# Optimization experiments

Hardware: AMD Instinct MI355X
Metric: run time of the kernel (lower is better)

## Reference

```python
import jax, jax.numpy as jnp
import numpy as np

BETA = 100.0
EXTS = [("r1", 515, 32, 16), ("r1_1", 512, 32, 16), ("r2", 512, 48, 12), ("r2_2", 576, 48, 12),
        ("r3", 576, 64, 12), ("r3_3", 768, 96, 8), ("r4", 768, 128, 6), ("r4_4", 768, 160, 6),
        ("r5", 960, 192, 5), ("r5_5", 960, 224, 4)]


def _wn(v, g):
    # torch weight_norm(dim=0): w[o] = g[o] * v[o] / ||v[o]||  (norm over input dims)
    n = jnp.sqrt(jnp.sum(v * v, axis=-1, keepdims=True))
    return g[..., None] * v / n


def _softplus_b(z):
    # torch Softplus(beta): (1/beta) * log(1 + exp(beta*z))
    return jax.nn.softplus(BETA * z) / BETA


def _resnext(x, grad, v, g, b):
    # x: [B,Cin,N], grad: [B,N,Cin,3]; v: [L,c,Cin] -- L parallel 1x1-conv branches,
    # outputs concatenated along channels (each branch reads the SAME input x).
    w = _wn(v, g)                                             # [L,c,Cin]
    pre = jnp.einsum('lci,bin->blcn', w, x) + b[None, :, :, None]
    sg = jax.nn.sigmoid(BETA * pre)                           # softplus' = sigmoid(beta*pre)
    B, L, c, N = pre.shape
    x_out = _softplus_b(pre).reshape(B, L * c, N)
    g_out = jnp.einsum('lci,bnid->bnlcd', w, grad)            # analytic chain-rule matmul
    g_out = (sg.transpose(0, 3, 1, 2)[..., None] * g_out).reshape(B, N, L * c, 3)
    return x_out, g_out


def setup_inputs() -> dict:
    key = jax.random.key(0)
    ks = iter(jax.random.split(key, 64))
    B, N = 1, 4096
    d = {}
    d["input"] = jax.random.normal(next(ks), (B, N, 3), jnp.float32)
    d["latent"] = jax.random.normal(next(ks), (B, 256), jnp.float32) * 0.1
    d["c1_v"] = jax.random.normal(next(ks), (515, 259), jnp.float32) * np.float32(np.sqrt(2.0 / 259.0))
    d["c1_g"] = 1.0 + 0.01 * jax.random.normal(next(ks), (515,), jnp.float32)
    d["c1_b"] = jnp.zeros((515,), jnp.float32)
    for name, cin, c, L in EXTS:
        d[name + "_v"] = jax.random.normal(next(ks), (L, c, cin), jnp.float32) * np.float32(np.sqrt(2.0 / cin))
        d[name + "_g"] = 1.0 + 0.01 * jax.random.normal(next(ks), (L, c), jnp.float32)
        d[name + "_b"] = jnp.zeros((L, c), jnp.float32)
    d["c10_v"] = jax.random.normal(next(ks), (1, 896), jnp.float32) * 1e-4 + np.float32(np.sqrt(np.pi / 896.0))
    d["c10_g"] = 1.0 + 0.01 * jax.random.normal(next(ks), (1,), jnp.float32)
    d["c10_b"] = -jnp.ones((1,), jnp.float32)
    return d


def reference(input, latent, c1_v, c1_g, c1_b,
              r1_v, r1_g, r1_b, r1_1_v, r1_1_g, r1_1_b,
              r2_v, r2_g, r2_b, r2_2_v, r2_2_g, r2_2_b,
              r3_v, r3_g, r3_b, r3_3_v, r3_3_g, r3_3_b,
              r4_v, r4_g, r4_b, r4_4_v, r4_4_g, r4_4_b,
              r5_v, r5_g, r5_b, r5_5_v, r5_5_g, r5_5_b,
              c10_v, c10_g, c10_b):
    # ImplicitMap_fExtrator.forward with compute_grad=True, cat_latent=True
    B, N = input.shape[0], input.shape[1]
    lat = jnp.broadcast_to(latent[:, None, :], (B, N, latent.shape[-1]))
    input_con = jnp.concatenate([input, lat], axis=-1)        # [B,N,259]
    x = input_con.transpose(0, 2, 1)                           # [B,259,N]

    # first conv: is_first=True -> input grad = w[:, :3] (d/d xyz)
    w1 = _wn(c1_v, c1_g)                                       # [515,259]
    pre = jnp.einsum('ci,bin->bcn', w1, x) + c1_b[None, :, None]
    grad = jnp.broadcast_to(w1[:, :3][None, None, :, :], (B, N, 515, 3))
    grad = jax.nn.sigmoid(BETA * pre).transpose(0, 2, 1)[..., None] * grad
    x = _softplus_b(pre)

    ext_params = [(r1_v, r1_g, r1_b), (r1_1_v, r1_1_g, r1_1_b),
                  (r2_v, r2_g, r2_b), (r2_2_v, r2_2_g, r2_2_b),
                  (r3_v, r3_g, r3_b), (r3_3_v, r3_3_g, r3_3_b),
                  (r4_v, r4_g, r4_b), (r4_4_v, r4_4_g, r4_4_b),
                  (r5_v, r5_g, r5_b), (r5_5_v, r5_5_g, r5_5_b)]
    for v, g, b in ext_params:
        x, grad = _resnext(x, grad, v, g, b)

    w10 = _wn(c10_v, c10_g)                                    # [1,896]
    out = jnp.einsum('ci,bin->bcn', w10, x) + c10_b[None, :, None]  # [B,1,N]
    out_grad = jnp.einsum('ci,bnid->bncd', w10, grad)               # [B,N,1,3]
    return out, out_grad, input_con
```

## Files before the change

kernel.cpp:

```cpp
#include <hip/hip_runtime.h>
#include <hip/hip_bf16.h>


#define NPTS 4096
#define XS 968

typedef unsigned short u16;
typedef unsigned int   u32;
typedef __attribute__((ext_vector_type(8))) __bf16 bf16x8;
typedef __attribute__((ext_vector_type(4))) float  f32x4;

__device__ __forceinline__ float bf2f(u16 h) {
  return __uint_as_float(((u32)h) << 16);
}
__device__ __forceinline__ u16 f2bf(float f) {
  u32 u = __float_as_uint(f);
  u += 0x7fff + ((u >> 16) & 1);
  return (u16)(u >> 16);
}

__device__ __forceinline__ void act_sp_sg(float pre, float& sp, float& sg) {
  float z = 100.f * pre;
  float e = __expf(-fabsf(z));
  float r = 1.f / (1.f + e);
  float l = __logf(1.f + e) * 0.01f;
  if (z >= 0.f) { sg = r;       sp = pre + l; }
  else          { sg = 1.f - r; sp = l; }
}

__global__ __launch_bounds__(256)
void build_x0(const float* __restrict__ inp, const float* __restrict__ lat,
              u16* __restrict__ x0, float* __restrict__ con) {
  const int n = blockIdx.x;
  for (int i = threadIdx.x; i < 320; i += 256) {
    float v = (i < 3) ? inp[n * 3 + i] : ((i < 259) ? lat[i - 3] : 0.f);
    x0[(size_t)n * 320 + i] = f2bf(v);
    if (i < 259) con[(size_t)n * 259 + i] = v;
  }
}

struct WLayer { const float* v; const float* g; int Cin, Cout, KS, MF; size_t woff; };
struct WAll { WLayer L[11]; };

__global__ __launch_bounds__(256)
void wnormF(WAll wa, u16* __restrict__ Wf) {
  const WLayer L = wa.L[blockIdx.y];
  const int cb = blockIdx.x;
  if (cb >= L.MF) return;
  __shared__ float red[16][17];
  __shared__ float scl[16];
  const int t = threadIdx.x;
  {
    const int col16 = t & 15, kt = t >> 4;
    const int col = cb * 16 + col16;
    float ss = 0.f;
    if (col < L.Cout)
      for (int k = kt; k < L.Cin; k += 16) {
        float x = L.v[(size_t)col * L.Cin + k]; ss += x * x;
      }
    red[col16][kt] = ss;
  }
  __syncthreads();
  if (t < 16) {
    float s = 0.f;
#pragma unroll
    for (int j = 0; j < 16; ++j) s += red[t][j];
    const int c = cb * 16 + t;
    scl[t] = (c < L.Cout) ? L.g[c] / sqrtf(s) : 0.f;
  }
  __syncthreads();
  u32* dst = (u32*)(Wf + L.woff);
  const int lane = t >> 2, q = t & 3;
  const int vcol = cb * 16 + (lane & 15);
  const float sc = scl[lane & 15];
  const float* vrow = L.v + (size_t)vcol * L.Cin;
  const bool cok = vcol < L.Cout;
  for (int ks = 0; ks < L.KS; ++ks) {
    const int k0 = ks * 32 + (lane >> 4) * 8 + q * 2;
    u16 lo = 0, hi16 = 0;
    if (cok) {
      if (k0 < L.Cin)     lo   = f2bf(vrow[k0] * sc);
      if (k0 + 1 < L.Cin) hi16 = f2bf(vrow[k0 + 1] * sc);
    }
    dst[(size_t)(ks * L.MF + cb) * 128 + t] = (u32)lo | ((u32)hi16 << 16);
  }
}

struct FusedArgs {
  size_t woff[11];
  const float* bias[11];
  const float* v10; const float* g10; const float* b10;
};

template<int KS, int MF, int COUT>
__device__ __forceinline__ void layer_mid(const u16* __restrict__ Wf,
                                          const float* __restrict__ bias,
                                          u16* __restrict__ X,
                                          int w, int lane, int lcol, int hi) {
  constexpr int NF = (MF + 11) / 12;
  f32x4 acc[4][NF];
#pragma unroll
  for (int s = 0; s < 4; ++s)
#pragma unroll
    for (int i = 0; i < NF; ++i) acc[s][i] = (f32x4){0.f, 0.f, 0.f, 0.f};

  const u16* wp = Wf + lane * 8;
  const int abase = lcol * XS + hi * 8;
  bf16x8 bA[NF], bB[NF];
#pragma unroll
  for (int i = 0; i < NF; ++i)
    if (w + 12 * i < MF)
      bA[i] = *(const bf16x8*)(wp + (size_t)(w + 12 * i) * 512);

#pragma unroll 1
  for (int ks = 0; ks < KS; ks += 2) {
    bf16x8 af[4];
#pragma unroll
    for (int s = 0; s < 4; ++s)
      af[s] = *(const bf16x8*)(X + abase + s * 16 * XS + ks * 32);
#pragma unroll
    for (int i = 0; i < NF; ++i)
      if (w + 12 * i < MF)
        bB[i] = *(const bf16x8*)(wp + (size_t)((ks + 1) * MF + w + 12 * i) * 512);
#pragma unroll
    for (int i = 0; i < NF; ++i)
      if (w + 12 * i < MF)
#pragma unroll
        for (int s = 0; s < 4; ++s)
          acc[s][i] = __builtin_amdgcn_mfma_f32_16x16x32_bf16(af[s], bA[i], acc[s][i], 0, 0, 0);
#pragma unroll
    for (int s = 0; s < 4; ++s)
      af[s] = *(const bf16x8*)(X + abase + s * 16 * XS + ks * 32 + 32);
    if (ks + 2 < KS) {
#pragma unroll
      for (int i = 0; i < NF; ++i)
        if (w + 12 * i < MF)
          bA[i] = *(const bf16x8*)(wp + (size_t)((ks + 2) * MF + w + 12 * i) * 512);
    }
#pragma unroll
    for (int i = 0; i < NF; ++i)
      if (w + 12 * i < MF)
#pragma unroll
        for (int s = 0; s < 4; ++s)
          acc[s][i] = __builtin_amdgcn_mfma_f32_16x16x32_bf16(af[s], bB[i], acc[s][i], 0, 0, 0);
  }
  __syncthreads();
#pragma unroll
  for (int i = 0; i < NF; ++i) {
    const int cb = w + 12 * i;
    if (cb < MF) {
      const int col = cb * 16 + lcol;
      const bool ok = col < COUT;
      const float bc = ok ? bias[col] : 0.f;
#pragma unroll
      for (int r = 0; r < 4; ++r) {
        const int p = hi * 4 + r;
        float sp = 0.f, sg = 0.f;
        if (ok) act_sp_sg(acc[0][i][r] + bc, sp, sg);
        X[(0 * 16 + p) * XS + col] = f2bf(sp);
        X[(1 * 16 + p) * XS + col] = f2bf(ok ? sg * acc[1][i][r] : 0.f);
        X[(2 * 16 + p) * XS + col] = f2bf(ok ? sg * acc[2][i][r] : 0.f);
        X[(3 * 16 + p) * XS + col] = f2bf(ok ? sg * acc[3][i][r] : 0.f);
      }
    }
  }
  __syncthreads();
}

template<int KS, int MF, int COUT>
__device__ __forceinline__ void layer_first(const u16* __restrict__ Wf,
                                            const float* __restrict__ bias,
                                            u16* __restrict__ X,
                                            int w, int lane, int lcol, int hi) {
  constexpr int NF = (MF + 11) / 12;
  f32x4 acc[NF];
#pragma unroll
  for (int i = 0; i < NF; ++i) acc[i] = (f32x4){0.f, 0.f, 0.f, 0.f};
  const u16* wp = Wf + lane * 8;
  const int abase = lcol * XS + hi * 8;
  bf16x8 bA[NF], bB[NF];
#pragma unroll
  for (int i = 0; i < NF; ++i)
    if (w + 12 * i < MF)
      bA[i] = *(const bf16x8*)(wp + (size_t)(w + 12 * i) * 512);
#pragma unroll 1
  for (int ks = 0; ks < KS; ks += 2) {
    bf16x8 af0 = *(const bf16x8*)(X + abase + ks * 32);
#pragma unroll
    for (int i = 0; i < NF; ++i)
      if (w + 12 * i < MF)
        bB[i] = *(const bf16x8*)(wp + (size_t)((ks + 1) * MF + w + 12 * i) * 512);
#pragma unroll
    for (int i = 0; i < NF; ++i)
      if (w + 12 * i < MF)
        acc[i] = __builtin_amdgcn_mfma_f32_16x16x32_bf16(af0, bA[i], acc[i], 0, 0, 0);
    bf16x8 af1 = *(const bf16x8*)(X + abase + ks * 32 + 32);
    if (ks + 2 < KS) {
#pragma unroll
      for (int i = 0; i < NF; ++i)
        if (w + 12 * i < MF)
          bA[i] = *(const bf16x8*)(wp + (size_t)((ks + 2) * MF + w + 12 * i) * 512);
    }
#pragma unroll
    for (int i = 0; i < NF; ++i)
      if (w + 12 * i < MF)
        acc[i] = __builtin_amdgcn_mfma_f32_16x16x32_bf16(af1, bB[i], acc[i], 0, 0, 0);
  }
  __syncthreads();
#pragma unroll
  for (int i = 0; i < NF; ++i) {
    const int cb = w + 12 * i;
    if (cb < MF) {
      const int col = cb * 16 + lcol;
      const bool ok = col < COUT;
      float bc = 0.f, w0 = 0.f, w1 = 0.f, w2 = 0.f;
      if (ok) {
        bc = bias[col];
        const u16* wk = Wf + ((size_t)cb * 64 + lcol) * 8;
        w0 = bf2f(wk[0]); w1 = bf2f(wk[1]); w2 = bf2f(wk[2]);
      }
#pragma unroll
      for (int r = 0; r < 4; ++r) {
        const int p = hi * 4 + r;
        float sp = 0.f, sg = 0.f;
        if (ok) act_sp_sg(acc[i][r] + bc, sp, sg);
        X[(0 * 16 + p) * XS + col] = f2bf(sp);
        X[(1 * 16 + p) * XS + col] = f2bf(sg * w0);
        X[(2 * 16 + p) * XS + col] = f2bf(sg * w1);
        X[(3 * 16 + p) * XS + col] = f2bf(sg * w2);
      }
    }
  }
  __syncthreads();
}

__global__ __launch_bounds__(768, 1)
void fused_net(FusedArgs fa, const u16* __restrict__ WfAll,
               const u16* __restrict__ x0,
               float* __restrict__ out, float* __restrict__ outg) {
  __shared__ __align__(16) u16 X[64 * XS];
  __shared__ float fred[12];
  const int t = threadIdx.x;
  const int w = t >> 6, lane = t & 63;
  const int lcol = lane & 15, hi = lane >> 4;
  const int n0 = blockIdx.x * 16;

  for (int c = t; c < 640; c += 768) {
    const int row = c / 40, ch = c % 40;
    uint4 q = *reinterpret_cast<const uint4*>(x0 + (size_t)(n0 + row) * 320 + ch * 8);
    *reinterpret_cast<uint4*>(X + row * XS + ch * 8) = q;
  }
  __syncthreads();

  layer_first<10, 36, 515>(WfAll + fa.woff[0],  fa.bias[0],  X, w, lane, lcol, hi);
  layer_mid<18, 32, 512>(WfAll + fa.woff[1],  fa.bias[1],  X, w, lane, lcol, hi);
  layer_mid<16, 32, 512>(WfAll + fa.woff[2],  fa.bias[2],  X, w, lane, lcol, hi);
  layer_mid<16, 36, 576>(WfAll + fa.woff[3],  fa.bias[3],  X, w, lane, lcol, hi);
  layer_mid<18, 36, 576>(WfAll + fa.woff[4],  fa.bias[4],  X, w, lane, lcol, hi);
  layer_mid<18, 48, 768>(WfAll + fa.woff[5],  fa.bias[5],  X, w, lane, lcol, hi);
  layer_mid<24, 48, 768>(WfAll + fa.woff[6],  fa.bias[6],  X, w, lane, lcol, hi);
  layer_mid<24, 48, 768>(WfAll + fa.woff[7],  fa.bias[7],  X, w, lane, lcol, hi);
  layer_mid<24, 60, 960>(WfAll + fa.woff[8],  fa.bias[8],  X, w, lane, lcol, hi);
  layer_mid<30, 60, 960>(WfAll + fa.woff[9],  fa.bias[9],  X, w, lane, lcol, hi);
  layer_mid<30, 56, 896>(WfAll + fa.woff[10], fa.bias[10], X, w, lane, lcol, hi);

  float ss = 0.f;
  for (int k = t; k < 896; k += 768) { float x = fa.v10[k]; ss += x * x; }
#pragma unroll
  for (int off = 32; off > 0; off >>= 1) ss += __shfl_xor(ss, off);
  if (lane == 0) fred[w] = ss;
  __syncthreads();
  float tot = 0.f;
#pragma unroll
  for (int j = 0; j < 12; ++j) tot += fred[j];
  const float scale = fa.g10[0] / sqrtf(tot);

  for (int id = w; id < 64; id += 12) {
    const int s = id >> 4, p = id & 15;
    const u16* xr = X + (s * 16 + p) * XS;
    float d = 0.f;
#pragma unroll
    for (int j = 0; j < 14; ++j) {
      const int k = lane * 14 + j;
      d += fa.v10[k] * bf2f(xr[k]);
    }
    d *= scale;
#pragma unroll
    for (int off = 32; off > 0; off >>= 1) d += __shfl_xor(d, off);
    if (lane == 0) {
      if (s == 0) out[n0 + p] = d + fa.b10[0];
      else        outg[(size_t)(n0 + p) * 3 + (s - 1)] = d;
    }
  }
}

extern "C" void kernel_launch(void* const* d_in, const int* in_sizes, int n_in,
                              void* d_out, int out_size, void* d_ws, size_t ws_size,
                              hipStream_t stream) {
  static const int CIN [11] = {259,515,512,512,576,576,768,768,768,960,960};
  static const int COUT[11] = {515,512,512,576,576,768,768,768,960,960,896};
  static const int KS  [11] = {10,18,16,16,18,18,24,24,24,30,30};
  static const int MF  [11] = {36,32,32,36,36,48,48,48,60,60,56};

  size_t woff[12]; woff[0] = 0;
  for (int l = 0; l < 11; ++l)
    woff[l + 1] = woff[l] + (size_t)KS[l] * MF[l] * 512;

  char* ws = (char*)d_ws;
  u16* Wf = (u16*)ws;
  size_t off = (woff[11] * 2 + 255) & ~(size_t)255;
  u16* x0 = (u16*)(ws + off);

  float* out_sdf  = (float*)d_out;
  float* out_grad = out_sdf + NPTS;
  float* out_con  = out_sdf + NPTS + NPTS*3;

  build_x0<<<dim3(NPTS), dim3(256), 0, stream>>>(
      (const float*)d_in[0], (const float*)d_in[1], x0, out_con);

  WAll wa;
  for (int l = 0; l < 11; ++l) {
    wa.L[l].v = (const float*)d_in[2 + 3 * l];
    wa.L[l].g = (const float*)d_in[3 + 3 * l];
    wa.L[l].Cin = CIN[l]; wa.L[l].Cout = COUT[l];
    wa.L[l].KS = KS[l]; wa.L[l].MF = MF[l];
    wa.L[l].woff = woff[l];
  }
  wnormF<<<dim3(60, 11), dim3(256), 0, stream>>>(wa, Wf);

  FusedArgs fa;
  for (int l = 0; l < 11; ++l) {
    fa.woff[l] = woff[l];
    fa.bias[l] = (const float*)d_in[4 + 3 * l];
  }
  fa.v10 = (const float*)d_in[35];
  fa.g10 = (const float*)d_in[36];
  fa.b10 = (const float*)d_in[37];

  fused_net<<<dim3(NPTS / 16), dim3(768), 0, stream>>>(
      fa, Wf, x0, out_sdf, out_grad);
}
```

Baseline: 225.9 us.

## Fold input build into fused kernel, add MFMA priority hints, fix wnorm access

Removes the separate build_x0 launch: the fused kernel now builds its bf16 input tile directly in shared memory and writes the concatenated output itself, which saves a launch and a workspace round trip. It also wraps the MFMA blocks in the mid layers with s_setprio so math waves get issue priority over loads. The weight-norm reduction now maps consecutive threads to consecutive k for coalesced reads. In exchange, the staging loop in the fused kernel does scalar, uncoalesced-ish work that the old separate kernel had spread across far more threads.

```diff
diff --git a/kernel.cpp b/kernel.cpp
--- a/kernel.cpp
+++ b/kernel.cpp
@@ -26,17 +26,6 @@
   float l = __logf(1.f + e) * 0.01f;
   if (z >= 0.f) { sg = r;       sp = pre + l; }
   else          { sg = 1.f - r; sp = l; }
-}
-
-__global__ __launch_bounds__(256)
-void build_x0(const float* __restrict__ inp, const float* __restrict__ lat,
-              u16* __restrict__ x0, float* __restrict__ con) {
-  const int n = blockIdx.x;
-  for (int i = threadIdx.x; i < 320; i += 256) {
-    float v = (i < 3) ? inp[n * 3 + i] : ((i < 259) ? lat[i - 3] : 0.f);
-    x0[(size_t)n * 320 + i] = f2bf(v);
-    if (i < 259) con[(size_t)n * 259 + i] = v;
-  }
 }
 
 struct WLayer { const float* v; const float* g; int Cin, Cout, KS, MF; size_t woff; };
@@ -51,7 +40,7 @@
   __shared__ float scl[16];
   const int t = threadIdx.x;
   {
-    const int col16 = t & 15, kt = t >> 4;
+    const int col16 = t >> 4, kt = t & 15;
     const int col = cb * 16 + col16;
     float ss = 0.f;
     if (col < L.Cout)
@@ -105,7 +94,7 @@
     for (int i = 0; i < NF; ++i) acc[s][i] = (f32x4){0.f, 0.f, 0.f, 0.f};
 
   const u16* wp = Wf + lane * 8;
-  const int abase = lcol * XS + hi * 8;
+  const u16* xa = X + lcol * XS + hi * 8;
   bf16x8 bA[NF], bB[NF];
 #pragma unroll
   for (int i = 0; i < NF; ++i)
@@ -117,32 +106,38 @@
     bf16x8 af[4];
 #pragma unroll
     for (int s = 0; s < 4; ++s)
-      af[s] = *(const bf16x8*)(X + abase + s * 16 * XS + ks * 32);
+      af[s] = *(const bf16x8*)(xa + s * 16 * XS + ks * 32);
 #pragma unroll
     for (int i = 0; i < NF; ++i)
       if (w + 12 * i < MF)
         bB[i] = *(const bf16x8*)(wp + (size_t)((ks + 1) * MF + w + 12 * i) * 512);
-#pragma unroll
-    for (int i = 0; i < NF; ++i)
-      if (w + 12 * i < MF)
+    __builtin_amdgcn_s_setprio(1);
+#pragma unroll
+    for (int i = 0; i < NF; ++i)
+      if (w + 12 * i < MF) {
 #pragma unroll
         for (int s = 0; s < 4; ++s)
           acc[s][i] = __builtin_amdgcn_mfma_f32_16x16x32_bf16(af[s], bA[i], acc[s][i], 0, 0, 0);
+      }
+    __builtin_amdgcn_s_setprio(0);
 #pragma unroll
     for (int s = 0; s < 4; ++s)
-      af[s] = *(const bf16x8*)(X + abase + s * 16 * XS + ks * 32 + 32);
+      af[s] = *(const bf16x8*)(xa + s * 16 * XS + ks * 32 + 32);
     if (ks + 2 < KS) {
 #pragma unroll
       for (int i = 0; i < NF; ++i)
         if (w + 12 * i < MF)
           bA[i] = *(const bf16x8*)(wp + (size_t)((ks + 2) * MF + w + 12 * i) * 512);
     }
-#pragma unroll
-    for (int i = 0; i < NF; ++i)
-      if (w + 12 * i < MF)
+    __builtin_amdgcn_s_setprio(1);
+#pragma unroll
+    for (int i = 0; i < NF; ++i)
+      if (w + 12 * i < MF) {
 #pragma unroll
         for (int s = 0; s < 4; ++s)
           acc[s][i] = __builtin_amdgcn_mfma_f32_16x16x32_bf16(af[s], bB[i], acc[s][i], 0, 0, 0);
+      }
+    __builtin_amdgcn_s_setprio(0);
   }
   __syncthreads();
 #pragma unroll
@@ -177,7 +172,7 @@
 #pragma unroll
   for (int i = 0; i < NF; ++i) acc[i] = (f32x4){0.f, 0.f, 0.f, 0.f};
   const u16* wp = Wf + lane * 8;
-  const int abase = lcol * XS + hi * 8;
+  const u16* xa = X + lcol * XS + hi * 8;
   bf16x8 bA[NF], bB[NF];
 #pragma unroll
   for (int i = 0; i < NF; ++i)
@@ -185,7 +180,7 @@
       bA[i] = *(const bf16x8*)(wp + (size_t)(w + 12 * i) * 512);
 #pragma unroll 1
   for (int ks = 0; ks < KS; ks += 2) {
-    bf16x8 af0 = *(const bf16x8*)(X + abase + ks * 32);
+    bf16x8 af0 = *(const bf16x8*)(xa + ks * 32);
 #pragma unroll
     for (int i = 0; i < NF; ++i)
       if (w + 12 * i < MF)
@@ -194,7 +189,7 @@
     for (int i = 0; i < NF; ++i)
       if (w + 12 * i < MF)
         acc[i] = __builtin_amdgcn_mfma_f32_16x16x32_bf16(af0, bA[i], acc[i], 0, 0, 0);
-    bf16x8 af1 = *(const bf16x8*)(X + abase + ks * 32 + 32);
+    bf16x8 af1 = *(const bf16x8*)(xa + ks * 32 + 32);
     if (ks + 2 < KS) {
 #pragma unroll
       for (int i = 0; i < NF; ++i)
@@ -236,8 +231,9 @@
 
 __global__ __launch_bounds__(768, 1)
 void fused_net(FusedArgs fa, const u16* __restrict__ WfAll,
-               const u16* __restrict__ x0,
-               float* __restrict__ out, float* __restrict__ outg) {
+               const float* __restrict__ inp, const float* __restrict__ lat,
+               float* __restrict__ out, float* __restrict__ outg,
+               float* __restrict__ con) {
   __shared__ __align__(16) u16 X[64 * XS];
   __shared__ float fred[12];
   const int t = threadIdx.x;
@@ -245,10 +241,12 @@
   const int lcol = lane & 15, hi = lane >> 4;
   const int n0 = blockIdx.x * 16;
 
-  for (int c = t; c < 640; c += 768) {
-    const int row = c / 40, ch = c % 40;
-    uint4 q = *reinterpret_cast<const uint4*>(x0 + (size_t)(n0 + row) * 320 + ch * 8);
-    *reinterpret_cast<uint4*>(X + row * XS + ch * 8) = q;
+  for (int c = t; c < 16 * 320; c += 768) {
+    const int row = c / 320, i = c - row * 320;
+    const float v = (i < 3) ? inp[(size_t)(n0 + row) * 3 + i]
+                  : ((i < 259) ? lat[i - 3] : 0.f);
+    X[row * XS + i] = f2bf(v);
+    if (i < 259) con[(size_t)(n0 + row) * 259 + i] = v;
   }
   __syncthreads();
 
@@ -306,17 +304,11 @@
   for (int l = 0; l < 11; ++l)
     woff[l + 1] = woff[l] + (size_t)KS[l] * MF[l] * 512;
 
-  char* ws = (char*)d_ws;
-  u16* Wf = (u16*)ws;
-  size_t off = (woff[11] * 2 + 255) & ~(size_t)255;
-  u16* x0 = (u16*)(ws + off);
+  u16* Wf = (u16*)d_ws;
 
   float* out_sdf  = (float*)d_out;
   float* out_grad = out_sdf + NPTS;
   float* out_con  = out_sdf + NPTS + NPTS*3;
-
-  build_x0<<<dim3(NPTS), dim3(256), 0, stream>>>(
-      (const float*)d_in[0], (const float*)d_in[1], x0, out_con);
 
   WAll wa;
   for (int l = 0; l < 11; ++l) {
@@ -338,5 +330,6 @@
   fa.b10 = (const float*)d_in[37];
 
   fused_net<<<dim3(NPTS / 16), dim3(768), 0, stream>>>(
-      fa, Wf, x0, out_sdf, out_grad);
-}
+      fa, Wf, (const float*)d_in[0], (const float*)d_in[1],
+      out_sdf, out_grad, out_con);
+}
```

Measured after the change: 219.8 us. -2.7%, faster.
